# Kernel tuning notes

Measured on AMD Instinct MI355X. Metric: run time of the kernel, lower is better.

The kernel has to match this reference:

```python
import jax, jax.numpy as jnp
import numpy as np

G, P = 128, 32          # num scenes, peds per scene
H, E = 64, 64           # h_dim, embedding_dim_pooling
D1, D2 = 512, 1024      # mlp_pre_pool dims
EPS = 1e-5


def setup_inputs() -> dict:
    key = jax.random.key(0)
    ks = jax.random.split(key, 16)
    N = G * P
    starts = jnp.arange(G, dtype=jnp.int64) * P
    seq_start_end = jnp.stack([starts, starts + P], axis=1)
    def lin(k, fin, fout):
        kw, kb = jax.random.split(k)
        s = 1.0 / np.sqrt(fin)
        return (jax.random.uniform(kw, (fin, fout), jnp.float32, -s, s),
                jax.random.uniform(kb, (fout,), jnp.float32, -s, s))
    Ws, bs = lin(ks[0], 2, E)
    Wv, bv = lin(ks[1], 1, E)
    W1, b1 = lin(ks[2], 3 * E, D1)
    W2, b2 = lin(ks[3], D1, D2)
    return {
        "h_states": jax.random.normal(ks[4], (N, H), jnp.float32),
        "seq_start_end": seq_start_end,
        "end_pos": jax.random.normal(ks[5], (N, 2), jnp.float32),
        "end_pos_speed": jax.random.uniform(ks[6], (N, 1), jnp.float32),
        "Ws": Ws, "bs": bs, "Wv": Wv, "bv": bv,
        "W1": W1, "b1": b1, "g1": jnp.ones((D1,), jnp.float32), "be1": jnp.zeros((D1,), jnp.float32),
        "W2": W2, "b2": b2, "g2": jnp.ones((D2,), jnp.float32), "be2": jnp.zeros((D2,), jnp.float32),
    }


def _bn(h, gamma, beta):
    # BatchNorm1d in train mode, stats over the per-group edge batch (axes 1,2)
    m = h.mean(axis=(1, 2), keepdims=True)
    v = ((h - m) ** 2).mean(axis=(1, 2), keepdims=True)  # biased variance
    return (h - m) * jax.lax.rsqrt(v + EPS) * gamma + beta


def reference(h_states, seq_start_end, end_pos, end_pos_speed,
              Ws, bs, Wv, bv, W1, b1, g1, be1, W2, b2, g2, be2):
    g = seq_start_end.shape[0]
    p = h_states.shape[0] // g
    pos = end_pos.reshape(g, p, 2)
    spd = end_pos_speed.reshape(g, p, 1)
    hid = h_states.reshape(g, p, H)
    # edge (i, j): rel = pos[j] - pos[i]; features of j for hidden & speed
    rel = pos[:, None, :, :] - pos[:, :, None, :]          # [G,P(i),P(j),2]
    rel_e = rel @ Ws + bs                                   # [G,P,P,E]
    spd_e = spd @ Wv + bv                                   # [G,P,E]
    hid_b = jnp.broadcast_to(hid[:, None, :, :], (g, p, p, H))
    spd_b = jnp.broadcast_to(spd_e[:, None, :, :], (g, p, p, E))
    x = jnp.concatenate([rel_e, hid_b, spd_b], axis=-1)     # [G,P,P,3E]
    h1 = jax.nn.relu(_bn(x @ W1 + b1, g1, be1))             # [G,P,P,512]
    h2 = jax.nn.relu(_bn(h1 @ W2 + b2, g2, be2))            # [G,P,P,1024]
    pooled = h2.max(axis=2)                                 # max over j
    return pooled.reshape(g * p, -1)
```

## Files before the change

### kernel.cpp

```cpp
#include <hip/hip_runtime.h>
#include <cstdint>

typedef unsigned short ushort_t;
typedef __attribute__((ext_vector_type(8))) __bf16 bf16x8;
typedef __attribute__((ext_vector_type(4))) float f32x4;
typedef __attribute__((ext_vector_type(4))) int i32x4;

#define NG 128
#define NP 32
#define NH 64
#define ND1 512
#define ND2 1024

__device__ inline ushort_t f2bf(float f) {
    uint32_t u = __float_as_uint(f);
    uint32_t r = (u + 0x7FFFu + ((u >> 16) & 1u)) >> 16;
    return (ushort_t)r;
}

#define GLL16(gp, lp) __builtin_amdgcn_global_load_lds( \
    (const __attribute__((address_space(1))) unsigned int*)(gp), \
    (__attribute__((address_space(3))) unsigned int*)(lp), 16, 0, 0)

__global__ void k0_prep(const float* __restrict__ Ws, const float* __restrict__ bs,
                        const float* __restrict__ Wv, const float* __restrict__ bv,
                        const float* __restrict__ W1, const float* __restrict__ b1,
                        float* __restrict__ Mws, float* __restrict__ uo, float* __restrict__ vo) {
    int ch = threadIdx.x;
    float m0 = 0.f, m1 = 0.f, uu = 0.f, vv = b1[ch];
    for (int e = 0; e < 64; e++) {
        float w1a = W1[e * ND1 + ch];
        float w1c = W1[(128 + e) * ND1 + ch];
        m0 += Ws[e] * w1a;
        m1 += Ws[64 + e] * w1a;
        uu += Wv[e] * w1c;
        vv += bs[e] * w1a + bv[e] * w1c;
    }
    Mws[ch] = m0; Mws[ND1 + ch] = m1; uo[ch] = uu; vo[ch] = vv;
}

__global__ void k0b_w2t(const float* __restrict__ W2, ushort_t* __restrict__ W2T) {
    __shared__ ushort_t tile[64][65];
    int kb = blockIdx.x & 7, nb = blockIdx.x >> 3;
    int t = threadIdx.x;
    #pragma unroll
    for (int e = 0; e < 16; e++) {
        int lin = t + e * 256;
        int k = lin >> 6, n = lin & 63;
        tile[k][n] = f2bf(W2[(kb * 64 + k) * ND2 + nb * 64 + n]);
    }
    __syncthreads();
    #pragma unroll
    for (int e = 0; e < 16; e++) {
        int lin = t + e * 256;
        int k = lin & 63, n = lin >> 6;
        W2T[(nb * 64 + n) * ND1 + kb * 64 + k] = tile[k][n];
    }
}

__global__ void k2_group(const float* __restrict__ hstates, const float* __restrict__ pos,
                         const float* __restrict__ spd, const float* __restrict__ W1,
                         const float* __restrict__ g1, const float* __restrict__ be1,
                         const float* __restrict__ Mws, const float* __restrict__ uo,
                         const float* __restrict__ vo,
                         float* __restrict__ u1, float* __restrict__ w1) {
    __shared__ float hid_s[32][64];
    __shared__ float pos_s[32][2];
    __shared__ float spd_s[32];
    int g = blockIdx.x >> 1;
    int ch = ((blockIdx.x & 1) << 8) + threadIdx.x;
    for (int t = threadIdx.x; t < 2048; t += 256) hid_s[t >> 6][t & 63] = hstates[g * 2048 + t];
    if (threadIdx.x < 64) pos_s[threadIdx.x >> 1][threadIdx.x & 1] = pos[g * 64 + threadIdx.x];
    if (threadIdx.x < 32) spd_s[threadIdx.x] = spd[g * 32 + threadIdx.x];
    __syncthreads();
    float m0 = Mws[ch], m1 = Mws[ND1 + ch], uu = uo[ch], vv = vo[ch];
    float cj[32], qj[32];
    #pragma unroll
    for (int j = 0; j < 32; j++) {
        qj[j] = pos_s[j][0] * m0 + pos_s[j][1] * m1;
        cj[j] = vv + spd_s[j] * uu;
    }
    for (int h = 0; h < 64; h++) {
        float w = W1[(64 + h) * ND1 + ch];
        #pragma unroll
        for (int j = 0; j < 32; j++) cj[j] += hid_s[j][h] * w;
    }
    float S1 = 0.f, S2 = 0.f, C1 = 0.f, Cq = 0.f, C2 = 0.f;
    #pragma unroll
    for (int j = 0; j < 32; j++) {
        S1 += qj[j]; S2 += qj[j] * qj[j];
        C1 += cj[j]; Cq += cj[j] * qj[j]; C2 += cj[j] * cj[j];
    }
    float mean = C1 * (1.0f / 32.0f);
    float sumsq = 64.f * S2 - 2.f * S1 * S1 + 64.f * Cq - 2.f * S1 * C1 + 32.f * C2;
    float var = sumsq * (1.0f / 1024.0f) - mean * mean;
    float A1 = rsqrtf(var + 1e-5f) * g1[ch];
    float B1 = be1[ch] - mean * A1;
    #pragma unroll
    for (int j = 0; j < 32; j++) {
        u1[(g * 32 + j) * ND1 + ch] = (qj[j] + cj[j]) * A1 + B1;
        w1[(g * 32 + j) * ND1 + ch] = qj[j] * A1;
    }
}

__global__ void k2b_h1(const float* __restrict__ u1c, const float* __restrict__ w1c,
                       ushort_t* __restrict__ h1) {
    int t = blockIdx.x * 256 + threadIdx.x;
    int k8 = t & 63;
    int row = t >> 6;
    int gc = row >> 10, rem = row & 1023;
    int i = rem >> 5, j = rem & 31;
    const float4* pu = reinterpret_cast<const float4*>(u1c + (size_t)(gc * 32 + j) * ND1 + k8 * 8);
    const float4* pw = reinterpret_cast<const float4*>(w1c + (size_t)(gc * 32 + i) * ND1 + k8 * 8);
    float4 ua = pu[0], ub = pu[1], wa = pw[0], wb = pw[1];
    uint32_t p0 = (uint32_t)f2bf(fmaxf(ua.x - wa.x, 0.f)) | ((uint32_t)f2bf(fmaxf(ua.y - wa.y, 0.f)) << 16);
    uint32_t p1 = (uint32_t)f2bf(fmaxf(ua.z - wa.z, 0.f)) | ((uint32_t)f2bf(fmaxf(ua.w - wa.w, 0.f)) << 16);
    uint32_t p2 = (uint32_t)f2bf(fmaxf(ub.x - wb.x, 0.f)) | ((uint32_t)f2bf(fmaxf(ub.y - wb.y, 0.f)) << 16);
    uint32_t p3 = (uint32_t)f2bf(fmaxf(ub.z - wb.z, 0.f)) | ((uint32_t)f2bf(fmaxf(ub.w - wb.w, 0.f)) << 16);
    i32x4 v = {(int)p0, (int)p1, (int)p2, (int)p3};
    *reinterpret_cast<i32x4*>(h1 + (size_t)row * ND1 + k8 * 8) = v;
}

__global__ void kz_zero(float* __restrict__ p, int n) {
    int t = blockIdx.x * 256 + threadIdx.x;
    if (t < n) p[t] = 0.f;
}

__global__ __launch_bounds__(256, 2) void k3_gemm(
        const ushort_t* __restrict__ h1, const ushort_t* __restrict__ W2T,
        float* __restrict__ maxv, float* __restrict__ minv,
        float* __restrict__ psum, float* __restrict__ psq, int g0) {
    __shared__ __align__(16) ushort_t a_lds[128 * 32];
    __shared__ __align__(16) ushort_t b_lds[128 * 32];
    int b = blockIdx.x;
    int mt = (b & 7) + ((b >> 6) << 3);
    int nt = (b >> 3) & 7;
    int tid = threadIdx.x;
    int w = tid >> 6, l = tid & 63;
    int wm = w >> 1, wn = w & 1;
    int lo = l & 15, lhi = l >> 4;

    const char* Ag = reinterpret_cast<const char*>(h1) + (size_t)mt * 128 * ND1 * 2;
    const char* Bg = reinterpret_cast<const char*>(W2T) + (size_t)nt * 128 * ND1 * 2;
    int soff0 = (w * 32 + (l >> 2)) * 1024 + (l & 3) * 16;
    int soff1 = soff0 + 16 * 1024;
    char* alds0 = reinterpret_cast<char*>(a_lds) + (w * 2 + 0) * 1024;
    char* alds1 = reinterpret_cast<char*>(a_lds) + (w * 2 + 1) * 1024;
    char* blds0 = reinterpret_cast<char*>(b_lds) + (w * 2 + 0) * 1024;
    char* blds1 = reinterpret_cast<char*>(b_lds) + (w * 2 + 1) * 1024;

    f32x4 acc[4][4];
    #pragma unroll
    for (int a = 0; a < 4; a++)
        #pragma unroll
        for (int c = 0; c < 4; c++) acc[a][c] = (f32x4){0.f, 0.f, 0.f, 0.f};

    int aoff = (wm * 64 + lo) * 64 + lhi * 16;
    int boff = (wn * 64 + lo) * 64 + lhi * 16;

    for (int kt = 0; kt < 16; kt++) {
        int kb = kt * 64;
        GLL16(Ag + soff0 + kb, alds0);
        GLL16(Ag + soff1 + kb, alds1);
        GLL16(Bg + soff0 + kb, blds0);
        GLL16(Bg + soff1 + kb, blds1);
        __syncthreads();
        bf16x8 af[4], bfv[4];
        #pragma unroll
        for (int fr = 0; fr < 4; fr++)
            af[fr] = *reinterpret_cast<const bf16x8*>(reinterpret_cast<const char*>(a_lds) + aoff + fr * 1024);
        #pragma unroll
        for (int fc = 0; fc < 4; fc++)
            bfv[fc] = *reinterpret_cast<const bf16x8*>(reinterpret_cast<const char*>(b_lds) + boff + fc * 1024);
        #pragma unroll
        for (int fr = 0; fr < 4; fr++)
            #pragma unroll
            for (int fc = 0; fc < 4; fc++)
                acc[fr][fc] = __builtin_amdgcn_mfma_f32_16x16x32_bf16(af[fr], bfv[fc], acc[fr][fc], 0, 0, 0);
        __syncthreads();
    }

    int g = g0 + (mt >> 3);
    int ib = ((mt & 7) << 2) + wm * 2;
    #pragma unroll
    for (int fc = 0; fc < 4; fc++) {
        int col = nt * 128 + wn * 64 + fc * 16 + lo;
        float mx0 = -1e30f, mn0 = 1e30f, mx1 = -1e30f, mn1 = 1e30f, sm = 0.f, sq = 0.f;
        #pragma unroll
        for (int fr = 0; fr < 2; fr++)
            #pragma unroll
            for (int r = 0; r < 4; r++) {
                float y = acc[fr][fc][r];
                mx0 = fmaxf(mx0, y); mn0 = fminf(mn0, y);
                sm += y; sq += y * y;
            }
        #pragma unroll
        for (int fr = 2; fr < 4; fr++)
            #pragma unroll
            for (int r = 0; r < 4; r++) {
                float y = acc[fr][fc][r];
                mx1 = fmaxf(mx1, y); mn1 = fminf(mn1, y);
                sm += y; sq += y * y;
            }
        #pragma unroll
        for (int mask = 16; mask < 64; mask <<= 1) {
            mx0 = fmaxf(mx0, __shfl_xor(mx0, mask, 64));
            mn0 = fminf(mn0, __shfl_xor(mn0, mask, 64));
            mx1 = fmaxf(mx1, __shfl_xor(mx1, mask, 64));
            mn1 = fminf(mn1, __shfl_xor(mn1, mask, 64));
            sm += __shfl_xor(sm, mask, 64);
            sq += __shfl_xor(sq, mask, 64);
        }
        if (lhi == 0) {
            size_t i0 = (size_t)(g * 32 + ib) * ND2 + col;
            maxv[i0] = mx0; minv[i0] = mn0;
            maxv[i0 + ND2] = mx1; minv[i0 + ND2] = mn1;
            atomicAdd(&psum[g * ND2 + col], sm);
            atomicAdd(&psq[g * ND2 + col], sq);
        }
    }
}

__global__ void k4_final(const float* __restrict__ maxv, const float* __restrict__ minv,
                         const float* __restrict__ psum, const float* __restrict__ psq,
                         const float* __restrict__ b2, const float* __restrict__ g2,
                         const float* __restrict__ be2, float* __restrict__ out) {
    int g = blockIdx.x >> 2;
    int col = ((blockIdx.x & 3) << 8) + threadIdx.x;
    float b2v = b2[col];
    float s = psum[g * ND2 + col] * (1.f / 1024.f);
    float q = psq[g * ND2 + col] * (1.f / 1024.f);
    float mean = s + b2v;
    float var = q + 2.f * b2v * s + b2v * b2v - mean * mean;
    float A2 = rsqrtf(var + 1e-5f) * g2[col];
    float B2 = be2[col] - mean * A2;
    for (int i = 0; i < 32; i++) {
        size_t idx = (size_t)(g * 32 + i) * ND2 + col;
        float y = ((A2 >= 0.f) ? maxv[idx] : minv[idx]) + b2v;
        out[idx] = fmaxf(y * A2 + B2, 0.f);
    }
}

extern "C" void kernel_launch(void* const* d_in, const int* in_sizes, int n_in,
                              void* d_out, int out_size, void* d_ws, size_t ws_size,
                              hipStream_t stream) {
    (void)in_sizes; (void)n_in; (void)out_size;
    const float* h_states = (const float*)d_in[0];
    const float* end_pos  = (const float*)d_in[2];
    const float* end_spd  = (const float*)d_in[3];
    const float* Ws  = (const float*)d_in[4];
    const float* bs  = (const float*)d_in[5];
    const float* Wv  = (const float*)d_in[6];
    const float* bv  = (const float*)d_in[7];
    const float* W1  = (const float*)d_in[8];
    const float* b1  = (const float*)d_in[9];
    const float* g1  = (const float*)d_in[10];
    const float* be1 = (const float*)d_in[11];
    const float* W2  = (const float*)d_in[12];
    const float* b2  = (const float*)d_in[13];
    const float* g2  = (const float*)d_in[14];
    const float* be2 = (const float*)d_in[15];
    float* ws = (float*)d_ws;
    float* Mws  = ws + 0;
    float* uo   = ws + 1024;
    float* vo   = ws + 1536;
    float* u1   = ws + 2048;
    float* w1x  = ws + 2099200;
    ushort_t* W2T = (ushort_t*)(ws + 4196352);
    float* maxv = ws + 4458496;
    float* minv = ws + 8652800;
    float* psum = ws + 12847104;
    float* psq  = ws + 12978176;
    ushort_t* h1 = (ushort_t*)(ws + 13109248);
    float* out = (float*)d_out;

    const size_t fixed_f = 13109248ULL;
    int CG = 128;
    while (CG > 4 && (fixed_f + (size_t)CG * 262144ULL) * 4ULL > ws_size) CG >>= 1;
    int nch = 128 / CG;

    hipLaunchKernelGGL(k0_prep, dim3(1), dim3(512), 0, stream, Ws, bs, Wv, bv, W1, b1, Mws, uo, vo);
    hipLaunchKernelGGL(k0b_w2t, dim3(128), dim3(256), 0, stream, W2, W2T);
    hipLaunchKernelGGL(k2_group, dim3(256), dim3(256), 0, stream,
                       h_states, end_pos, end_spd, W1, g1, be1, Mws, uo, vo, u1, w1x);
    hipLaunchKernelGGL(kz_zero, dim3(1024), dim3(256), 0, stream, psum, 262144);
    for (int c = 0; c < nch; c++) {
        const float* u1c = u1 + (size_t)c * CG * 32 * ND1;
        const float* w1c = w1x + (size_t)c * CG * 32 * ND1;
        hipLaunchKernelGGL(k2b_h1, dim3(CG * 256), dim3(256), 0, stream, u1c, w1c, h1);
        hipLaunchKernelGGL(k3_gemm, dim3(CG * 64), dim3(256), 0, stream,
                           h1, W2T, maxv, minv, psum, psq, c * CG);
    }
    hipLaunchKernelGGL(k4_final, dim3(512), dim3(256), 0, stream,
                       maxv, minv, psum, psq, b2, g2, be2, out);
}
```

Before: 338.2 us.

## Merge prep kernels and use K=64 XOR-swizzled LDS tiles in GEMM

Folds the weight prep, W2 transpose, per-group BN1 kernel and psum zeroing into one launch, so each BN1 block recomputes the small projection vectors itself. The GEMM now stages 64-wide K tiles, halving the number of barrier-separated iterations. h1 and W2T are written in an XOR-swizzled layout so the fragment reads from LDS avoid bank conflicts. This costs double the LDS per block, which may lower occupancy, and adds redundant prep arithmetic in each block.

```diff
diff --git a/kernel.cpp b/kernel.cpp
--- a/kernel.cpp
+++ b/kernel.cpp
@@ -22,84 +22,84 @@
     (const __attribute__((address_space(1))) unsigned int*)(gp), \
     (__attribute__((address_space(3))) unsigned int*)(lp), 16, 0, 0)
 
-__global__ void k0_prep(const float* __restrict__ Ws, const float* __restrict__ bs,
-                        const float* __restrict__ Wv, const float* __restrict__ bv,
-                        const float* __restrict__ W1, const float* __restrict__ b1,
-                        float* __restrict__ Mws, float* __restrict__ uo, float* __restrict__ vo) {
-    int ch = threadIdx.x;
-    float m0 = 0.f, m1 = 0.f, uu = 0.f, vv = b1[ch];
-    for (int e = 0; e < 64; e++) {
-        float w1a = W1[e * ND1 + ch];
-        float w1c = W1[(128 + e) * ND1 + ch];
-        m0 += Ws[e] * w1a;
-        m1 += Ws[64 + e] * w1a;
-        uu += Wv[e] * w1c;
-        vv += bs[e] * w1a + bv[e] * w1c;
-    }
-    Mws[ch] = m0; Mws[ND1 + ch] = m1; uo[ch] = uu; vo[ch] = vv;
-}
-
-__global__ void k0b_w2t(const float* __restrict__ W2, ushort_t* __restrict__ W2T) {
-    __shared__ ushort_t tile[64][65];
-    int kb = blockIdx.x & 7, nb = blockIdx.x >> 3;
-    int t = threadIdx.x;
-    #pragma unroll
-    for (int e = 0; e < 16; e++) {
-        int lin = t + e * 256;
-        int k = lin >> 6, n = lin & 63;
-        tile[k][n] = f2bf(W2[(kb * 64 + k) * ND2 + nb * 64 + n]);
-    }
-    __syncthreads();
-    #pragma unroll
-    for (int e = 0; e < 16; e++) {
-        int lin = t + e * 256;
-        int k = lin & 63, n = lin >> 6;
-        W2T[(nb * 64 + n) * ND1 + kb * 64 + k] = tile[k][n];
-    }
-}
-
-__global__ void k2_group(const float* __restrict__ hstates, const float* __restrict__ pos,
-                         const float* __restrict__ spd, const float* __restrict__ W1,
-                         const float* __restrict__ g1, const float* __restrict__ be1,
-                         const float* __restrict__ Mws, const float* __restrict__ uo,
-                         const float* __restrict__ vo,
-                         float* __restrict__ u1, float* __restrict__ w1) {
+__global__ void k2_all(const float* __restrict__ hstates, const float* __restrict__ pos,
+                       const float* __restrict__ spd, const float* __restrict__ W1,
+                       const float* __restrict__ g1, const float* __restrict__ be1,
+                       const float* __restrict__ Ws, const float* __restrict__ bs,
+                       const float* __restrict__ Wv, const float* __restrict__ bv,
+                       const float* __restrict__ b1, const float* __restrict__ W2,
+                       ushort_t* __restrict__ W2T,
+                       float* __restrict__ u1, float* __restrict__ w1,
+                       float* __restrict__ psum) {
     __shared__ float hid_s[32][64];
     __shared__ float pos_s[32][2];
     __shared__ float spd_s[32];
-    int g = blockIdx.x >> 1;
-    int ch = ((blockIdx.x & 1) << 8) + threadIdx.x;
-    for (int t = threadIdx.x; t < 2048; t += 256) hid_s[t >> 6][t & 63] = hstates[g * 2048 + t];
-    if (threadIdx.x < 64) pos_s[threadIdx.x >> 1][threadIdx.x & 1] = pos[g * 64 + threadIdx.x];
-    if (threadIdx.x < 32) spd_s[threadIdx.x] = spd[g * 32 + threadIdx.x];
-    __syncthreads();
-    float m0 = Mws[ch], m1 = Mws[ND1 + ch], uu = uo[ch], vv = vo[ch];
-    float cj[32], qj[32];
-    #pragma unroll
-    for (int j = 0; j < 32; j++) {
-        qj[j] = pos_s[j][0] * m0 + pos_s[j][1] * m1;
-        cj[j] = vv + spd_s[j] * uu;
-    }
-    for (int h = 0; h < 64; h++) {
-        float w = W1[(64 + h) * ND1 + ch];
-        #pragma unroll
-        for (int j = 0; j < 32; j++) cj[j] += hid_s[j][h] * w;
-    }
-    float S1 = 0.f, S2 = 0.f, C1 = 0.f, Cq = 0.f, C2 = 0.f;
-    #pragma unroll
-    for (int j = 0; j < 32; j++) {
-        S1 += qj[j]; S2 += qj[j] * qj[j];
-        C1 += cj[j]; Cq += cj[j] * qj[j]; C2 += cj[j] * cj[j];
-    }
-    float mean = C1 * (1.0f / 32.0f);
-    float sumsq = 64.f * S2 - 2.f * S1 * S1 + 64.f * Cq - 2.f * S1 * C1 + 32.f * C2;
-    float var = sumsq * (1.0f / 1024.0f) - mean * mean;
-    float A1 = rsqrtf(var + 1e-5f) * g1[ch];
-    float B1 = be1[ch] - mean * A1;
-    #pragma unroll
-    for (int j = 0; j < 32; j++) {
-        u1[(g * 32 + j) * ND1 + ch] = (qj[j] + cj[j]) * A1 + B1;
-        w1[(g * 32 + j) * ND1 + ch] = qj[j] * A1;
+    __shared__ ushort_t tile[64][65];
+    int b = blockIdx.x, tid = threadIdx.x;
+    if (b < 256) {
+        int t0 = b * 256 + tid;
+        #pragma unroll
+        for (int z = 0; z < 4; z++) psum[t0 + z * 65536] = 0.f;
+        int g = b >> 1;
+        int ch = ((b & 1) << 8) + tid;
+        for (int t = tid; t < 2048; t += 256) hid_s[t >> 6][t & 63] = hstates[g * 2048 + t];
+        if (tid < 64) pos_s[tid >> 1][tid & 1] = pos[g * 64 + tid];
+        if (tid < 32) spd_s[tid] = spd[g * 32 + tid];
+        float m0 = 0.f, m1 = 0.f, uu = 0.f, vv = b1[ch];
+        for (int e = 0; e < 64; e++) {
+            float w1a = W1[e * ND1 + ch];
+            float w1c = W1[(128 + e) * ND1 + ch];
+            m0 += Ws[e] * w1a;
+            m1 += Ws[64 + e] * w1a;
+            uu += Wv[e] * w1c;
+            vv += bs[e] * w1a + bv[e] * w1c;
+        }
+        __syncthreads();
+        float cj[32], qj[32];
+        #pragma unroll
+        for (int j = 0; j < 32; j++) {
+            qj[j] = pos_s[j][0] * m0 + pos_s[j][1] * m1;
+            cj[j] = vv + spd_s[j] * uu;
+        }
+        for (int h = 0; h < 64; h++) {
+            float w = W1[(64 + h) * ND1 + ch];
+            #pragma unroll
+            for (int j = 0; j < 32; j++) cj[j] += hid_s[j][h] * w;
+        }
+        float S1 = 0.f, S2 = 0.f, C1 = 0.f, Cq = 0.f, C2 = 0.f;
+        #pragma unroll
+        for (int j = 0; j < 32; j++) {
+            S1 += qj[j]; S2 += qj[j] * qj[j];
+            C1 += cj[j]; Cq += cj[j] * qj[j]; C2 += cj[j] * cj[j];
+        }
+        float mean = C1 * (1.0f / 32.0f);
+        float sumsq = 64.f * S2 - 2.f * S1 * S1 + 64.f * Cq - 2.f * S1 * C1 + 32.f * C2;
+        float var = sumsq * (1.0f / 1024.0f) - mean * mean;
+        float A1 = rsqrtf(var + 1e-5f) * g1[ch];
+        float B1 = be1[ch] - mean * A1;
+        #pragma unroll
+        for (int j = 0; j < 32; j++) {
+            u1[(g * 32 + j) * ND1 + ch] = (qj[j] + cj[j]) * A1 + B1;
+            w1[(g * 32 + j) * ND1 + ch] = qj[j] * A1;
+        }
+    } else {
+        int tb = b - 256;
+        int kb2 = tb & 7, nb = tb >> 3;
+        #pragma unroll
+        for (int e = 0; e < 16; e++) {
+            int lin = tid + e * 256;
+            int k = lin >> 6, n = lin & 63;
+            tile[k][n] = f2bf(W2[(kb2 * 64 + k) * ND2 + nb * 64 + n]);
+        }
+        __syncthreads();
+        #pragma unroll
+        for (int e = 0; e < 16; e++) {
+            int lin = tid + e * 256;
+            int kl = lin & 63, nl = lin >> 6;
+            int n = nb * 64 + nl, k = kb2 * 64 + kl;
+            int idx = n * ND1 + ((k >> 6) << 6) + (((((k >> 3) & 7) ^ (n & 7))) << 3) + (k & 7);
+            W2T[idx] = tile[kl][nl];
+        }
     }
 }
 
@@ -118,20 +118,16 @@
     uint32_t p2 = (uint32_t)f2bf(fmaxf(ub.x - wb.x, 0.f)) | ((uint32_t)f2bf(fmaxf(ub.y - wb.y, 0.f)) << 16);
     uint32_t p3 = (uint32_t)f2bf(fmaxf(ub.z - wb.z, 0.f)) | ((uint32_t)f2bf(fmaxf(ub.w - wb.w, 0.f)) << 16);
     i32x4 v = {(int)p0, (int)p1, (int)p2, (int)p3};
-    *reinterpret_cast<i32x4*>(h1 + (size_t)row * ND1 + k8 * 8) = v;
-}
-
-__global__ void kz_zero(float* __restrict__ p, int n) {
-    int t = blockIdx.x * 256 + threadIdx.x;
-    if (t < n) p[t] = 0.f;
+    int kt = k8 >> 3, c = k8 & 7;
+    *reinterpret_cast<i32x4*>(h1 + (size_t)row * ND1 + (kt << 6) + (((c ^ (row & 7))) << 3)) = v;
 }
 
 __global__ __launch_bounds__(256, 2) void k3_gemm(
         const ushort_t* __restrict__ h1, const ushort_t* __restrict__ W2T,
         float* __restrict__ maxv, float* __restrict__ minv,
         float* __restrict__ psum, float* __restrict__ psq, int g0) {
-    __shared__ __align__(16) ushort_t a_lds[128 * 32];
-    __shared__ __align__(16) ushort_t b_lds[128 * 32];
+    __shared__ __align__(16) ushort_t a_lds[128 * 64];
+    __shared__ __align__(16) ushort_t b_lds[128 * 64];
     int b = blockIdx.x;
     int mt = (b & 7) + ((b >> 6) << 3);
     int nt = (b >> 3) & 7;
@@ -142,12 +138,9 @@
 
     const char* Ag = reinterpret_cast<const char*>(h1) + (size_t)mt * 128 * ND1 * 2;
     const char* Bg = reinterpret_cast<const char*>(W2T) + (size_t)nt * 128 * ND1 * 2;
-    int soff0 = (w * 32 + (l >> 2)) * 1024 + (l & 3) * 16;
-    int soff1 = soff0 + 16 * 1024;
-    char* alds0 = reinterpret_cast<char*>(a_lds) + (w * 2 + 0) * 1024;
-    char* alds1 = reinterpret_cast<char*>(a_lds) + (w * 2 + 1) * 1024;
-    char* blds0 = reinterpret_cast<char*>(b_lds) + (w * 2 + 0) * 1024;
-    char* blds1 = reinterpret_cast<char*>(b_lds) + (w * 2 + 1) * 1024;
+    int gbase = (w * 32 + (l >> 3)) * 1024 + (l & 7) * 16;
+    char* aldsb = reinterpret_cast<char*>(a_lds) + w * 4096;
+    char* bldsb = reinterpret_cast<char*>(b_lds) + w * 4096;
 
     f32x4 acc[4][4];
     #pragma unroll
@@ -155,28 +148,38 @@
         #pragma unroll
         for (int c = 0; c < 4; c++) acc[a][c] = (f32x4){0.f, 0.f, 0.f, 0.f};
 
-    int aoff = (wm * 64 + lo) * 64 + lhi * 16;
-    int boff = (wn * 64 + lo) * 64 + lhi * 16;
-
-    for (int kt = 0; kt < 16; kt++) {
-        int kb = kt * 64;
-        GLL16(Ag + soff0 + kb, alds0);
-        GLL16(Ag + soff1 + kb, alds1);
-        GLL16(Bg + soff0 + kb, blds0);
-        GLL16(Bg + soff1 + kb, blds1);
-        __syncthreads();
-        bf16x8 af[4], bfv[4];
-        #pragma unroll
-        for (int fr = 0; fr < 4; fr++)
-            af[fr] = *reinterpret_cast<const bf16x8*>(reinterpret_cast<const char*>(a_lds) + aoff + fr * 1024);
-        #pragma unroll
-        for (int fc = 0; fc < 4; fc++)
-            bfv[fc] = *reinterpret_cast<const bf16x8*>(reinterpret_cast<const char*>(b_lds) + boff + fc * 1024);
-        #pragma unroll
-        for (int fr = 0; fr < 4; fr++)
-            #pragma unroll
-            for (int fc = 0; fc < 4; fc++)
-                acc[fr][fc] = __builtin_amdgcn_mfma_f32_16x16x32_bf16(af[fr], bfv[fc], acc[fr][fc], 0, 0, 0);
+    for (int kt = 0; kt < 8; kt++) {
+        int kb = kt * 128;
+        #pragma unroll
+        for (int q = 0; q < 4; q++) {
+            GLL16(Ag + gbase + q * 8192 + kb, aldsb + q * 1024);
+            GLL16(Bg + gbase + q * 8192 + kb, bldsb + q * 1024);
+        }
+        __syncthreads();
+        bf16x8 af[4][2], bfv[4][2];
+        #pragma unroll
+        for (int fr = 0; fr < 4; fr++) {
+            int r = wm * 64 + fr * 16 + lo;
+            #pragma unroll
+            for (int kc = 0; kc < 2; kc++)
+                af[fr][kc] = *reinterpret_cast<const bf16x8*>(
+                    reinterpret_cast<const char*>(a_lds) + r * 128 + (((kc * 4 + lhi) ^ (r & 7)) << 4));
+        }
+        #pragma unroll
+        for (int fc = 0; fc < 4; fc++) {
+            int r = wn * 64 + fc * 16 + lo;
+            #pragma unroll
+            for (int kc = 0; kc < 2; kc++)
+                bfv[fc][kc] = *reinterpret_cast<const bf16x8*>(
+                    reinterpret_cast<const char*>(b_lds) + r * 128 + (((kc * 4 + lhi) ^ (r & 7)) << 4));
+        }
+        #pragma unroll
+        for (int kc = 0; kc < 2; kc++)
+            #pragma unroll
+            for (int fr = 0; fr < 4; fr++)
+                #pragma unroll
+                for (int fc = 0; fc < 4; fc++)
+                    acc[fr][fc] = __builtin_amdgcn_mfma_f32_16x16x32_bf16(af[fr][kc], bfv[fc][kc], acc[fr][fc], 0, 0, 0);
         __syncthreads();
     }
 
@@ -261,9 +264,6 @@
     const float* g2  = (const float*)d_in[14];
     const float* be2 = (const float*)d_in[15];
     float* ws = (float*)d_ws;
-    float* Mws  = ws + 0;
-    float* uo   = ws + 1024;
-    float* vo   = ws + 1536;
     float* u1   = ws + 2048;
     float* w1x  = ws + 2099200;
     ushort_t* W2T = (ushort_t*)(ws + 4196352);
@@ -279,11 +279,9 @@
     while (CG > 4 && (fixed_f + (size_t)CG * 262144ULL) * 4ULL > ws_size) CG >>= 1;
     int nch = 128 / CG;
 
-    hipLaunchKernelGGL(k0_prep, dim3(1), dim3(512), 0, stream, Ws, bs, Wv, bv, W1, b1, Mws, uo, vo);
-    hipLaunchKernelGGL(k0b_w2t, dim3(128), dim3(256), 0, stream, W2, W2T);
-    hipLaunchKernelGGL(k2_group, dim3(256), dim3(256), 0, stream,
-                       h_states, end_pos, end_spd, W1, g1, be1, Mws, uo, vo, u1, w1x);
-    hipLaunchKernelGGL(kz_zero, dim3(1024), dim3(256), 0, stream, psum, 262144);
+    hipLaunchKernelGGL(k2_all, dim3(384), dim3(256), 0, stream,
+                       h_states, end_pos, end_spd, W1, g1, be1,
+                       Ws, bs, Wv, bv, b1, W2, W2T, u1, w1x, psum);
     for (int c = 0; c < nch; c++) {
         const float* u1c = u1 + (size_t)c * CG * 32 * ND1;
         const float* w1c = w1x + (size_t)c * CG * 32 * ND1;
```

New measurement: 325.1 us. 1.04x faster.
